# Kernel optimization log

Hardware: AMD Instinct MI355X
Metric: run time of the kernel (lower is better)

The kernel has to match this reference:

```python
import jax, jax.numpy as jnp
import numpy as np
import math

D = 256; H = 8; L = 6; DK = D // H

def _ln(x, g, b):
    m = jnp.mean(x, -1, keepdims=True)
    v = jnp.mean((x - m) ** 2, -1, keepdims=True)
    return (x - m) * jax.lax.rsqrt(v + 1e-5) * g + b

def setup_inputs() -> dict:
    key = jax.random.key(0)
    ks = jax.random.split(key, 16)
    B, N, F, E = 8, 768, 128, 4
    s = 0.02
    inp = {}
    inp['node_feats'] = jax.random.normal(ks[0], (B, N, F), jnp.float32)
    inp['adj'] = jax.random.randint(ks[1], (B, N, N), 0, 2, jnp.int32)
    inp['dist'] = jax.random.uniform(ks[2], (B, N, N), jnp.float32)
    inp['edge_type_oh'] = jax.random.uniform(ks[3], (B, N, N, E), jnp.float32)
    inp['node_proj_w'] = jax.random.normal(ks[4], (F, D), jnp.float32) * s
    inp['node_proj_b'] = jnp.zeros((D,), jnp.float32)
    inp['cls'] = jax.random.normal(ks[5], (1, 1, D), jnp.float32) * s
    inp['etw'] = jax.random.normal(ks[6], (E,), jnp.float32) * s
    inp['noedge_bias'] = jnp.float32(-2.0)
    inp['deg_scale'] = jnp.float32(0.2)
    inp['gamma'] = jnp.float32(0.8)
    inp['v2n'] = jnp.float32(0.1)
    inp['n2v'] = jnp.float32(0.1)
    inp['vself'] = jnp.float32(0.05)
    inp['ln1_g'] = jnp.ones((L, D), jnp.float32); inp['ln1_b'] = jnp.zeros((L, D), jnp.float32)
    inp['qw'] = jax.random.normal(ks[7], (L, D, D), jnp.float32) * s; inp['qb'] = jnp.zeros((L, D), jnp.float32)
    inp['kw'] = jax.random.normal(ks[8], (L, D, D), jnp.float32) * s; inp['kb'] = jnp.zeros((L, D), jnp.float32)
    inp['vw'] = jax.random.normal(ks[9], (L, D, D), jnp.float32) * s; inp['vb'] = jnp.zeros((L, D), jnp.float32)
    inp['ow'] = jax.random.normal(ks[10], (L, D, D), jnp.float32) * s; inp['ob'] = jnp.zeros((L, D), jnp.float32)
    inp['ln2_g'] = jnp.ones((L, D), jnp.float32); inp['ln2_b'] = jnp.zeros((L, D), jnp.float32)
    Dm = int(D * 1.0)  # mlp_ratio=1.0
    inp['fc1w'] = jax.random.normal(ks[11], (L, D, Dm), jnp.float32) * s; inp['fc1b'] = jnp.zeros((L, Dm), jnp.float32)
    inp['fc2w'] = jax.random.normal(ks[12], (L, Dm, D), jnp.float32) * s; inp['fc2b'] = jnp.zeros((L, D), jnp.float32)
    return inp

def _build_bias(adj_f, dist, edge_type_oh, etw, noedge_bias, deg_scale, gamma, v2n, n2v, vself):
    # DynamicAttnBiasBuilder: hard_mask=False, use_degree=True, vnode_spd_mode='replace', gamma != 0
    B, N, _ = adj_f.shape
    T = N + 1
    e = jnp.einsum('bije,e->bij', edge_type_oh, etw) - gamma * dist  # (B,N,N)
    e = jnp.where(adj_f > 0, e, e + noedge_bias)
    deg = adj_f.sum(-1)  # (B,N)
    deg_norm = (deg[:, :, None] + deg[:, None, :]) / (deg.max(axis=1, keepdims=True)[:, :, None] + 1e-6)
    e = e + deg_scale * deg_norm
    bias = jnp.zeros((B, T, T), jnp.float32)
    bias = bias.at[:, 1:, 1:].set(e)
    bias = bias.at[:, 0, 1:].set(v2n)   # vnode_spd_mode == 'replace'
    bias = bias.at[:, 1:, 0].set(n2v)
    bias = bias.at[:, 0, 0].set(vself)
    return bias  # (B,T,T), broadcast over heads

def _mhsa(x, bias, qw, qb, kw, kb, vw, vb, ow, ob):
    B, T, _ = x.shape
    q = (x @ qw + qb).reshape(B, T, H, DK).transpose(0, 2, 1, 3)
    k = (x @ kw + kb).reshape(B, T, H, DK).transpose(0, 2, 1, 3)
    v = (x @ vw + vb).reshape(B, T, H, DK).transpose(0, 2, 1, 3)
    scores = jnp.einsum('bhqd,bhkd->bhqk', q, k) / math.sqrt(DK)
    scores = scores + bias[:, None, :, :]
    attn = jax.nn.softmax(scores, axis=-1)
    out = jnp.einsum('bhqk,bhkd->bhqd', attn, v)
    out = out.transpose(0, 2, 1, 3).reshape(B, T, D)
    return out @ ow + ob

def _forward(node_feats, adj, dist, edge_type_oh, node_proj_w, node_proj_b, cls,
             etw, noedge_bias, deg_scale, gamma, v2n, n2v, vself,
             ln1_g, ln1_b, qw, qb, kw, kb, vw, vb, ow, ob,
             ln2_g, ln2_b, fc1w, fc1b, fc2w, fc2b):
    adj_f = adj.astype(jnp.float32)
    bias = _build_bias(adj_f, dist, edge_type_oh, etw, noedge_bias, deg_scale, gamma, v2n, n2v, vself)
    B = node_feats.shape[0]
    x = node_feats @ node_proj_w + node_proj_b  # (B,N,D)
    x = jnp.concatenate([jnp.broadcast_to(cls, (B, 1, D)), x], axis=1)  # prepend virtual node -> (B,T,D)
    for l in range(L):
        h = _mhsa(_ln(x, ln1_g[l], ln1_b[l]), bias, qw[l], qb[l], kw[l], kb[l], vw[l], vb[l], ow[l], ob[l])
        x = x + h
        m = _ln(x, ln2_g[l], ln2_b[l])
        m = jax.nn.gelu(m @ fc1w[l] + fc1b[l], approximate=False) @ fc2w[l] + fc2b[l]
        x = x + m
    return x

def reference(node_feats, adj, dist, edge_type_oh, node_proj_w, node_proj_b, cls,
              etw, noedge_bias, deg_scale, gamma, v2n, n2v, vself,
              ln1_g, ln1_b, qw, qb, kw, kb, vw, vb, ow, ob,
              ln2_g, ln2_b, fc1w, fc1b, fc2w, fc2b):
    return _forward(node_feats, adj, dist, edge_type_oh, node_proj_w, node_proj_b, cls,
                    etw, noedge_bias, deg_scale, gamma, v2n, n2v, vself,
                    ln1_g, ln1_b, qw, qb, kw, kb, vw, vb, ow, ob,
                    ln2_g, ln2_b, fc1w, fc1b, fc2w, fc2b)
```

## Files before the change

kernel.cpp:

```cpp
#include <hip/hip_runtime.h>
#include <math.h>

#define BB 8
#define NN 768
#define TT 769
#define DD 256
#define HH 8
#define DKK 32
#define FF 128
#define LL 6
#define MM 6152
#define SCALE 0.17677669529663687f
#define TP 832
#define KQP 784
#define KHS (KQP * DKK)
#define GBP 776
#define HP 264
#define WSZ 65536
#define NPK ((size_t)BB * 49 * 13 * 1024)

typedef __attribute__((ext_vector_type(8))) short s16x8;
typedef __attribute__((ext_vector_type(8))) unsigned short u16x8;
typedef __attribute__((ext_vector_type(4))) float f32x4;

__device__ inline short f2bf(float x) {
    unsigned u = __float_as_uint(x);
    unsigned r = (u + 0x7FFFu + ((u >> 16) & 1u)) >> 16;
    return (short)r;
}
__device__ inline float bf2f(unsigned short s) {
    return __uint_as_float(((unsigned)s) << 16);
}
__device__ inline float gelu_f(float x) {
    return 0.5f * x * (1.f + erff(x * 0.70710678118654752f));
}

__global__ __launch_bounds__(256) void deg_kernel(const int* __restrict__ adj,
                                                  float* __restrict__ deg) {
    int row  = blockIdx.x * 4 + (threadIdx.x >> 6);
    int lane = threadIdx.x & 63;
    const int* p = adj + (size_t)row * NN;
    int s = 0;
#pragma unroll
    for (int i = 0; i < NN / 64; ++i) s += p[lane + 64 * i];
#pragma unroll
    for (int off = 32; off > 0; off >>= 1) s += __shfl_xor(s, off);
    if (lane == 0) deg[row] = (float)s;
}

__global__ __launch_bounds__(256) void degmax_kernel(const float* __restrict__ deg,
                                                     float* __restrict__ dmax) {
    __shared__ float red[256];
    int b = blockIdx.x, t = threadIdx.x;
    float m = 0.f;
    for (int i = t; i < NN; i += 256) m = fmaxf(m, deg[b * NN + i]);
    red[t] = m;
    __syncthreads();
    for (int s = 128; s > 0; s >>= 1) {
        if (t < s) red[t] = fmaxf(red[t], red[t + s]);
        __syncthreads();
    }
    if (t == 0) dmax[b] = red[0];
}

__global__ __launch_bounds__(256) void bias_kernel(
    const float* __restrict__ dist, const float* __restrict__ eoh,
    const int* __restrict__ adj, const float* __restrict__ deg,
    const float* __restrict__ dmax, const float* __restrict__ etw,
    const float* __restrict__ noedge, const float* __restrict__ degsc,
    const float* __restrict__ gamma, const float* __restrict__ v2n,
    const float* __restrict__ n2v, const float* __restrict__ vself,
    unsigned short* __restrict__ bias)
{
    long long idx = (long long)blockIdx.x * 256 + threadIdx.x;
    const long long total = (long long)BB * TT * GBP;
    if (idx >= total) return;
    int b  = (int)(idx / ((long long)TT * GBP));
    int r  = (int)(idx % ((long long)TT * GBP));
    int qi = r / GBP, kj = r % GBP;
    float out;
    if (kj >= TT)                out = 0.f;
    else if (qi == 0 && kj == 0) out = vself[0];
    else if (qi == 0)            out = v2n[0];
    else if (kj == 0)            out = n2v[0];
    else {
        int i = qi - 1, j = kj - 1;
        size_t e = ((size_t)b * NN + i) * NN + j;
        float4 oh = *(const float4*)(eoh + 4 * e);
        float val = oh.x * etw[0] + oh.y * etw[1] + oh.z * etw[2] + oh.w * etw[3]
                    - gamma[0] * dist[e];
        if (adj[e] == 0) val += noedge[0];
        val += degsc[0] * (deg[b * NN + i] + deg[b * NN + j]) / (dmax[b] + 1e-6f);
        out = val;
    }
    bias[idx] = (unsigned short)f2bf(out);
}

__global__ __launch_bounds__(256) void biaspk_kernel(
    const unsigned short* __restrict__ bias, unsigned short* __restrict__ bpk)
{
    int idx = blockIdx.x * 256 + threadIdx.x;
    int jj   = idx & 7;
    int lane = (idx >> 3) & 63;
    int half = (idx >> 9) & 1;
    int c    = (idx >> 10) % 13;
    int qtb  = idx / (13 * 1024);
    int b = qtb / 49, qt = qtb - b * 49;
    int quad = lane >> 4, m16 = lane & 15;
    int j = half * 8 + jj, s = j >> 2, r = j & 3;
    int kj = c * 64 + s * 16 + m16; if (kj >= TT) kj = 0;
    int qi = qt * 16 + quad * 4 + r; if (qi >= TT) qi = TT - 1;
    bpk[idx] = bias[(size_t)(b * TT + qi) * GBP + kj];
}

__global__ __launch_bounds__(256) void nodeproj_ln_kernel(
    const float* __restrict__ nf, const float* __restrict__ w,
    const float* __restrict__ bsv, const float* __restrict__ cls,
    const float* __restrict__ g, const float* __restrict__ bvec,
    float* __restrict__ x, short* __restrict__ xn)
{
    __shared__ float sf[FF];
    __shared__ float red[256];
    int row = blockIdx.x, t = threadIdx.x;
    int b = row / TT, tr = row % TT;
    float y;
    if (tr == 0) {
        y = cls[t];
    } else {
        if (t < FF) sf[t] = nf[((size_t)b * NN + tr - 1) * FF + t];
        __syncthreads();
        y = bsv[t];
#pragma unroll 8
        for (int kk = 0; kk < FF; ++kk) y = fmaf(sf[kk], w[kk * DD + t], y);
    }
    x[(size_t)row * DD + t] = y;
    red[t] = y;
    __syncthreads();
    for (int s = 128; s > 0; s >>= 1) { if (t < s) red[t] += red[t + s]; __syncthreads(); }
    float mean = red[0] * (1.f / DD);
    __syncthreads();
    float d = y - mean;
    red[t] = d * d;
    __syncthreads();
    for (int s = 128; s > 0; s >>= 1) { if (t < s) red[t] += red[t + s]; __syncthreads(); }
    float var = red[0] * (1.f / DD);
    xn[(size_t)row * DD + t] = f2bf(d * rsqrtf(var + 1e-5f) * g[t] + bvec[t]);
}

__global__ __launch_bounds__(256) void wtrans_kernel(
    const float* __restrict__ qw, const float* __restrict__ kw,
    const float* __restrict__ vw, const float* __restrict__ ow,
    const float* __restrict__ f1w, const float* __restrict__ f2w,
    short* __restrict__ wt2)
{
    int mi = blockIdx.x >> 4, kg = blockIdx.x & 15;
    int fam = mi / 6, l = mi % 6;
    const float* W;
    if      (fam == 0) W = qw;
    else if (fam == 1) W = kw;
    else if (fam == 2) W = vw;
    else if (fam == 3) W = ow;
    else if (fam == 4) W = f1w;
    else               W = f2w;
    W += (size_t)l * DD * DD;
    int n = threadIdx.x;
    short* out = wt2 + (size_t)mi * WSZ;
#pragma unroll
    for (int kk = 0; kk < 16; ++kk) {
        int k = kg * 16 + kk;
        float val = W[(size_t)k * DD + n];
        size_t idx = (size_t)(((n >> 4) * 8 + (k >> 5)) * 512
                   + (((k >> 3) & 3) * 16 + (n & 15)) * 8 + (k & 7));
        out[idx] = f2bf(val);
    }
}

__global__ __launch_bounds__(256) void gemm_qkv_kernel(
    const short* __restrict__ A, const short* __restrict__ wtl,
    const float* __restrict__ qb, const float* __restrict__ kb,
    const float* __restrict__ vb,
    short* __restrict__ qh, short* __restrict__ kh, short* __restrict__ vtb)
{
    int t = threadIdx.x;
    int w = t >> 6, lane = t & 63, quad = lane >> 4, m16 = lane & 15;
    int bx = blockIdx.x;
    int bb = bx & 7, qt = bx >> 3;
    int fam = blockIdx.y;
    const short* Wf = wtl + (size_t)fam * 6 * WSZ;
    const float* bsv = fam == 0 ? qb : (fam == 1 ? kb : vb);
    int tpa = qt * 16 + m16; if (tpa >= TT) tpa = TT - 1;
    const short* ap = A + (size_t)(bb * TT + tpa) * DD + quad * 8;
    const short* wbase = Wf + (size_t)(w * 4) * 4096 + lane * 8;
    f32x4 acc[4] = {};
#pragma unroll
    for (int kc = 0; kc < 8; ++kc) {
        s16x8 af = *(const s16x8*)(ap + kc * 32);
#pragma unroll
        for (int nt = 0; nt < 4; ++nt) {
            s16x8 bf = *(const s16x8*)(wbase + (size_t)nt * 4096 + kc * 512);
            acc[nt] = __builtin_amdgcn_mfma_f32_16x16x32_bf16(af, bf, acc[nt], 0, 0, 0);
        }
    }
    if (fam < 2) {
        short* outp = fam == 0 ? qh : kh;
#pragma unroll
        for (int r = 0; r < 4; ++r) {
            int tpos = qt * 16 + quad * 4 + r;
            if (tpos < TT) {
                size_t rb = ((size_t)bb * HH * KQP + tpos) * DKK;
#pragma unroll
                for (int nt = 0; nt < 4; ++nt) {
                    int col = w * 64 + nt * 16 + m16;
                    float bv = bsv[col];
                    int h = col >> 5, dk = col & 31;
                    outp[rb + (size_t)h * KHS + dk] = f2bf(acc[nt][r] + bv);
                }
            }
        }
    } else {
#pragma unroll
        for (int nt = 0; nt < 4; ++nt) {
            int col = w * 64 + nt * 16 + m16;
            float bv = bsv[col];
            int h = col >> 5, dk = col & 31;
#pragma unroll
            for (int r = 0; r < 4; ++r) {
                int tpos = qt * 16 + quad * 4 + r;
                if (tpos < TT)
                    vtb[(((size_t)(bb * HH + h)) * DKK + dk) * TP + tpos] =
                        f2bf(acc[nt][r] + bv);
            }
        }
    }
}

__global__ __launch_bounds__(512) void mega_kernel(
    const short* __restrict__ q, const short* __restrict__ k,
    const short* __restrict__ vt, const unsigned short* __restrict__ bpk,
    const short* __restrict__ Wo, const short* __restrict__ W1,
    const short* __restrict__ W2,
    const float* __restrict__ ob, const float* __restrict__ g2,
    const float* __restrict__ b2, const float* __restrict__ f1b,
    const float* __restrict__ f2b, float* __restrict__ x,
    short* __restrict__ xn, const float* __restrict__ g1,
    const float* __restrict__ b1, int donext)
{
    __shared__ short Pb[8][16][72];
    __shared__ short xa[16][HP];
    __shared__ short xnl[16][HP];
    __shared__ short hb[16][HP];
    __shared__ float redS[16][8], redQ[16][8];

    int t = threadIdx.x;
    int w = t >> 6, lane = t & 63;
    int quad = lane >> 4, m16 = lane & 15;
    int bx = blockIdx.x;
    int b = bx & 7;
    int qt = bx >> 3;
    int h = w;
    int q0 = qt * 16;
    size_t qtb13 = (size_t)(b * 49 + qt) * 13;

    int qrow = q0 + m16;
    int qc = qrow < TT ? qrow : TT - 1;
    const short* qbase = q + (size_t)(b * HH + h) * KHS;
    s16x8 qa = *(const s16x8*)(qbase + (size_t)qc * DKK + quad * 8);

    const short* kbase = k + (size_t)(b * HH + h) * KHS;
    const short* vbase = vt + (((size_t)(b * HH + h)) * DKK) * TP;

    s16x8 kfA[4], kfB[4], vfA[4], vfB[4];
    u16x8 bbA0, bbA1, bbB0, bbB1;
    f32x4 sacc[4];
    f32x4 o0 = {0.f, 0.f, 0.f, 0.f};
    f32x4 o1 = {0.f, 0.f, 0.f, 0.f};
    float ls[4] = {0.f, 0.f, 0.f, 0.f};

#define LOADK_(DST, CC)                                                         \
    {                                                                           \
        _Pragma("unroll") for (int s = 0; s < 4; ++s) {                         \
            int kr = (CC) * 64 + s * 16 + m16;                                  \
            int kcl = kr < TT ? kr : TT - 1;                                    \
            DST[s] = *(const s16x8*)(kbase + (size_t)kcl * DKK + quad * 8);     \
        }                                                                       \
    }
#define LOADV_(DST, CC)                                                         \
    {                                                                           \
        int jn = (CC) * 64;                                                     \
        DST[0] = *(const s16x8*)(vbase + (size_t)m16 * TP + jn + quad * 8);     \
        DST[1] = *(const s16x8*)(vbase + (size_t)m16 * TP + jn + 32 + quad * 8);\
        DST[2] = *(const s16x8*)(vbase + (size_t)(16 + m16) * TP + jn + quad * 8);\
        DST[3] = *(const s16x8*)(vbase + (size_t)(16 + m16) * TP + jn + 32 + quad * 8);\
    }
#define LOADB_(D0, D1, CC)                                                      \
    {                                                                           \
        const unsigned short* bp_ = bpk + ((qtb13 + (CC)) << 10);               \
        D0 = *(const u16x8*)(bp_ + (lane << 3));                                \
        D1 = *(const u16x8*)(bp_ + 512 + (lane << 3));                         \
    }
#define STEP_(C, KPRE, KUSE, VUSE, VPRE, BU0, BU1, BP0, BP1, PK, PV, PBF, DOQK) \
    {                                                                           \
        if (PK)  LOADK_(KPRE, (C) + 2);                                         \
        if (PV)  LOADV_(VPRE, (C) + 1);                                         \
        if (PBF) LOADB_(BP0, BP1, (C) + 1);                                     \
        int j0 = (C) * 64;                                                      \
        _Pragma("unroll") for (int s = 0; s < 4; ++s) {                         \
            int key = j0 + s * 16 + m16;                                        \
            int kv = key < TT;                                                  \
            _Pragma("unroll") for (int r = 0; r < 4; ++r) {                     \
                int j = s * 4 + r;                                              \
                float bv = bf2f(j < 8 ? (unsigned short)BU0[j]                  \
                                      : (unsigned short)BU1[j - 8]);            \
                float sval = kv ? fmaf(sacc[s][r], SCALE, bv) : -1e30f;         \
                float p = __expf(sval - 8.0f);                                  \
                ls[r] += p;                                                     \
                Pb[w][quad * 4 + r][s * 16 + m16] = f2bf(p);                    \
            }                                                                   \
        }                                                                       \
        if (DOQK) {                                                             \
            f32x4 z = {0.f, 0.f, 0.f, 0.f};                                     \
            _Pragma("unroll") for (int s = 0; s < 4; ++s)                       \
                sacc[s] = __builtin_amdgcn_mfma_f32_16x16x32_bf16(qa, KUSE[s], z, 0, 0, 0); \
        }                                                                       \
        s16x8 pa0 = *(const s16x8*)&Pb[w][m16][quad * 8];                       \
        s16x8 pa1 = *(const s16x8*)&Pb[w][m16][32 + quad * 8];                  \
        o0 = __builtin_amdgcn_mfma_f32_16x16x32_bf16(pa0, VUSE[0], o0, 0, 0, 0);\
        o0 = __builtin_amdgcn_mfma_f32_16x16x32_bf16(pa1, VUSE[1], o0, 0, 0, 0);\
        o1 = __builtin_amdgcn_mfma_f32_16x16x32_bf16(pa0, VUSE[2], o1, 0, 0, 0);\
        o1 = __builtin_amdgcn_mfma_f32_16x16x32_bf16(pa1, VUSE[3], o1, 0, 0, 0);\
    }

    LOADK_(kfA, 0);
    LOADK_(kfB, 1);
    LOADV_(vfA, 0);
    LOADB_(bbA0, bbA1, 0);
    {
        f32x4 z = {0.f, 0.f, 0.f, 0.f};
#pragma unroll
        for (int s = 0; s < 4; ++s)
            sacc[s] = __builtin_amdgcn_mfma_f32_16x16x32_bf16(qa, kfA[s], z, 0, 0, 0);
    }

    for (int cc = 0; cc < 5; ++cc) {
        STEP_(2 * cc,     kfA, kfB, vfA, vfB, bbA0, bbA1, bbB0, bbB1, 1, 1, 1, 1)
        STEP_(2 * cc + 1, kfB, kfA, vfB, vfA, bbB0, bbB1, bbA0, bbA1, 1, 1, 1, 1)
    }
    STEP_(10, kfA, kfB, vfA, vfB, bbA0, bbA1, bbB0, bbB1, 1, 1, 1, 1)
    STEP_(11, kfB, kfA, vfB, vfA, bbB0, bbB1, bbA0, bbA1, 0, 1, 1, 1)
    STEP_(12, kfA, kfB, vfA, vfB, bbA0, bbA1, bbB0, bbB1, 0, 0, 0, 0)

#undef STEP_
#undef LOADB_
#undef LOADV_
#undef LOADK_

#pragma unroll
    for (int r = 0; r < 4; ++r) {
        float l = ls[r];
#pragma unroll
        for (int off = 1; off < 16; off <<= 1) l += __shfl_xor(l, off);
        float inv = 1.f / l;
        int rl = quad * 4 + r;
        xa[rl][h * DKK + m16]      = f2bf(o0[r] * inv);
        xa[rl][h * DKK + 16 + m16] = f2bf(o1[r] * inv);
    }
    __syncthreads();

    const short* wob = Wo + (size_t)(w * 2) * 4096 + lane * 8;
    f32x4 acco[2] = {};
#pragma unroll
    for (int kc = 0; kc < 8; ++kc) {
        s16x8 af = *(const s16x8*)&xa[m16][kc * 32 + quad * 8];
#pragma unroll
        for (int ntl = 0; ntl < 2; ++ntl) {
            s16x8 bf = *(const s16x8*)(wob + (size_t)ntl * 4096 + kc * 512);
            acco[ntl] = __builtin_amdgcn_mfma_f32_16x16x32_bf16(af, bf, acco[ntl], 0, 0, 0);
        }
    }
    float vv[2][4], sr[4], q2[4];
#pragma unroll
    for (int r = 0; r < 4; ++r) { sr[r] = 0.f; q2[r] = 0.f; }
#pragma unroll
    for (int ntl = 0; ntl < 2; ++ntl) {
        int col = w * 32 + ntl * 16 + m16;
        float bv = ob[col];
#pragma unroll
        for (int r = 0; r < 4; ++r) {
            int row = q0 + quad * 4 + r; if (row >= TT) row = TT - 1;
            float v = acco[ntl][r] + bv + x[((size_t)(b * TT + row)) * DD + col];
            vv[ntl][r] = v; sr[r] += v; q2[r] += v * v;
        }
    }
#pragma unroll
    for (int r = 0; r < 4; ++r)
#pragma unroll
        for (int off = 1; off < 16; off <<= 1) {
            sr[r] += __shfl_xor(sr[r], off);
            q2[r] += __shfl_xor(q2[r], off);
        }
    if (m16 == 0) {
#pragma unroll
        for (int r = 0; r < 4; ++r) {
            redS[quad * 4 + r][w] = sr[r];
            redQ[quad * 4 + r][w] = q2[r];
        }
    }
    __syncthreads();

#pragma unroll
    for (int r = 0; r < 4; ++r) {
        int rl = quad * 4 + r;
        float fs = 0.f, fq = 0.f;
#pragma unroll
        for (int j = 0; j < 8; ++j) { fs += redS[rl][j]; fq += redQ[rl][j]; }
        float mean = fs * (1.f / DD);
        float var = fq * (1.f / DD) - mean * mean;
        float inv = rsqrtf(var + 1e-5f);
#pragma unroll
        for (int ntl = 0; ntl < 2; ++ntl) {
            int col = w * 32 + ntl * 16 + m16;
            xnl[rl][col] = f2bf((vv[ntl][r] - mean) * inv * g2[col] + b2[col]);
        }
    }
    __syncthreads();

    const short* w1b = W1 + (size_t)(w * 2) * 4096 + lane * 8;
    f32x4 acc1[2] = {};
#pragma unroll
    for (int kc = 0; kc < 8; ++kc) {
        s16x8 af = *(const s16x8*)&xnl[m16][kc * 32 + quad * 8];
#pragma unroll
        for (int ntl = 0; ntl < 2; ++ntl) {
            s16x8 bf = *(const s16x8*)(w1b + (size_t)ntl * 4096 + kc * 512);
            acc1[ntl] = __builtin_amdgcn_mfma_f32_16x16x32_bf16(af, bf, acc1[ntl], 0, 0, 0);
        }
    }
#pragma unroll
    for (int ntl = 0; ntl < 2; ++ntl) {
        int col = w * 32 + ntl * 16 + m16;
        float fb = f1b[col];
#pragma unroll
        for (int r = 0; r < 4; ++r)
            hb[quad * 4 + r][col] = f2bf(gelu_f(acc1[ntl][r] + fb));
    }
    __syncthreads();

    const short* w2b = W2 + (size_t)(w * 2) * 4096 + lane * 8;
    f32x4 acc2[2] = {};
#pragma unroll
    for (int kc = 0; kc < 8; ++kc) {
        s16x8 af = *(const s16x8*)&hb[m16][kc * 32 + quad * 8];
#pragma unroll
        for (int ntl = 0; ntl < 2; ++ntl) {
            s16x8 bf = *(const s16x8*)(w2b + (size_t)ntl * 4096 + kc * 512);
            acc2[ntl] = __builtin_amdgcn_mfma_f32_16x16x32_bf16(af, bf, acc2[ntl], 0, 0, 0);
        }
    }
#pragma unroll
    for (int r = 0; r < 4; ++r) { sr[r] = 0.f; q2[r] = 0.f; }
#pragma unroll
    for (int ntl = 0; ntl < 2; ++ntl) {
        int col = w * 32 + ntl * 16 + m16;
        float bv = f2b[col];
#pragma unroll
        for (int r = 0; r < 4; ++r) {
            float v = acc2[ntl][r] + bv + vv[ntl][r];
            vv[ntl][r] = v; sr[r] += v; q2[r] += v * v;
        }
    }
#pragma unroll
    for (int r = 0; r < 4; ++r)
#pragma unroll
        for (int off = 1; off < 16; off <<= 1) {
            sr[r] += __shfl_xor(sr[r], off);
            q2[r] += __shfl_xor(q2[r], off);
        }
    if (m16 == 0) {
#pragma unroll
        for (int r = 0; r < 4; ++r) {
            redS[quad * 4 + r][w] = sr[r];
            redQ[quad * 4 + r][w] = q2[r];
        }
    }
    __syncthreads();

#pragma unroll
    for (int r = 0; r < 4; ++r) {
        int rl = quad * 4 + r;
        int row = q0 + rl;
        float fs = 0.f, fq = 0.f;
#pragma unroll
        for (int j = 0; j < 8; ++j) { fs += redS[rl][j]; fq += redQ[rl][j]; }
        float mean = fs * (1.f / DD);
        float var = fq * (1.f / DD) - mean * mean;
        float inv = rsqrtf(var + 1e-5f);
        if (row < TT) {
            size_t grow = (size_t)(b * TT + row) * DD;
#pragma unroll
            for (int ntl = 0; ntl < 2; ++ntl) {
                int col = w * 32 + ntl * 16 + m16;
                float v = vv[ntl][r];
                x[grow + col] = v;
                if (donext)
                    xn[grow + col] = f2bf((v - mean) * inv * g1[col] + b1[col]);
            }
        }
    }
}

extern "C" void kernel_launch(void* const* d_in, const int* in_sizes, int n_in,
                              void* d_out, int out_size, void* d_ws, size_t ws_size,
                              hipStream_t stream)
{
    const float* node_feats = (const float*)d_in[0];
    const int*   adj        = (const int*)d_in[1];
    const float* dist       = (const float*)d_in[2];
    const float* eoh        = (const float*)d_in[3];
    const float* npw        = (const float*)d_in[4];
    const float* npb        = (const float*)d_in[5];
    const float* cls        = (const float*)d_in[6];
    const float* etw        = (const float*)d_in[7];
    const float* noedge     = (const float*)d_in[8];
    const float* degsc      = (const float*)d_in[9];
    const float* gamma      = (const float*)d_in[10];
    const float* v2n        = (const float*)d_in[11];
    const float* n2v        = (const float*)d_in[12];
    const float* vself      = (const float*)d_in[13];
    const float* ln1g = (const float*)d_in[14];
    const float* ln1b = (const float*)d_in[15];
    const float* qw   = (const float*)d_in[16];
    const float* qb   = (const float*)d_in[17];
    const float* kw   = (const float*)d_in[18];
    const float* kb   = (const float*)d_in[19];
    const float* vw   = (const float*)d_in[20];
    const float* vb   = (const float*)d_in[21];
    const float* ow   = (const float*)d_in[22];
    const float* ob   = (const float*)d_in[23];
    const float* ln2g = (const float*)d_in[24];
    const float* ln2b = (const float*)d_in[25];
    const float* f1w  = (const float*)d_in[26];
    const float* f1b  = (const float*)d_in[27];
    const float* f2w  = (const float*)d_in[28];
    const float* f2b  = (const float*)d_in[29];

    float* x  = (float*)d_out;
    char* ws = (char*)d_ws;
    size_t off = 0;
    unsigned short* bias = (unsigned short*)(ws + off); off += (size_t)BB * TT * GBP * 2;
    unsigned short* bpk  = (unsigned short*)(ws + off); off += NPK * 2;
    float* deg  = (float*)(ws + off); off += (size_t)BB * NN * 4;
    float* dmax = (float*)(ws + off); off += 64;
    short* xn16 = (short*)(ws + off); off += (size_t)MM * DD * 2;
    short* qhb  = (short*)(ws + off); off += (size_t)BB * HH * KQP * DKK * 2;
    short* khb  = (short*)(ws + off); off += (size_t)BB * HH * KQP * DKK * 2;
    short* vtb  = (short*)(ws + off); off += (size_t)BB * HH * DKK * TP * 2;
    short* wt2  = (short*)(ws + off); off += (size_t)36 * WSZ * 2;

    deg_kernel<<<(BB * NN) / 4, 256, 0, stream>>>(adj, deg);
    degmax_kernel<<<BB, 256, 0, stream>>>(deg, dmax);

    long long total = (long long)BB * TT * GBP;
    bias_kernel<<<(int)((total + 255) / 256), 256, 0, stream>>>(
        dist, eoh, adj, deg, dmax, etw, noedge, degsc, gamma, v2n, n2v, vself, bias);

    biaspk_kernel<<<(int)(NPK / 256), 256, 0, stream>>>(bias, bpk);

    nodeproj_ln_kernel<<<MM, 256, 0, stream>>>(node_feats, npw, npb, cls,
                                               ln1g, ln1b, x, xn16);

    wtrans_kernel<<<576, 256, 0, stream>>>(qw, kw, vw, ow, f1w, f2w, wt2);

    dim3 gqkv(392, 3);
    gemm_qkv_kernel<<<gqkv, 256, 0, stream>>>(xn16, wt2, qb, kb, vb,
                                              qhb, khb, vtb);

    for (int l = 0; l < LL; ++l) {
        size_t bo = (size_t)l * DD;
        int donext = (l + 1 < LL) ? 1 : 0;
        size_t bn = (size_t)(l + 1 < LL ? l + 1 : 0) * DD;
        mega_kernel<<<392, 512, 0, stream>>>(
            qhb, khb, vtb, bpk,
            wt2 + (size_t)(18 + l) * WSZ,
            wt2 + (size_t)(24 + l) * WSZ,
            wt2 + (size_t)(30 + l) * WSZ,
            ob + bo, ln2g + bo, ln2b + bo, f1b + bo, f2b + bo,
            x, xn16, ln1g + bn, ln1b + bn, donext);
        if (donext)
            gemm_qkv_kernel<<<gqkv, 256, 0, stream>>>(
                xn16, wt2 + (size_t)(l + 1) * WSZ,
                qb + bn, kb + bn, vb + bn, qhb, khb, vtb);
    }
}
```

Measured before the change: 662.8 us.

## Split attention key range across two wave groups in 1024-thread mega kernel

```diff
diff --git a/kernel.cpp b/kernel.cpp
--- a/kernel.cpp
+++ b/kernel.cpp
@@ -234,7 +234,7 @@
     }
 }
 
-__global__ __launch_bounds__(512) void mega_kernel(
+__global__ __launch_bounds__(1024) void mega_kernel(
     const short* __restrict__ q, const short* __restrict__ k,
     const short* __restrict__ vt, const unsigned short* __restrict__ bpk,
     const short* __restrict__ Wo, const short* __restrict__ W1,
@@ -245,11 +245,11 @@
     short* __restrict__ xn, const float* __restrict__ g1,
     const float* __restrict__ b1, int donext)
 {
-    __shared__ short Pb[8][16][72];
+    __shared__ short Pb[16][16][72];
     __shared__ short xa[16][HP];
     __shared__ short xnl[16][HP];
     __shared__ short hb[16][HP];
-    __shared__ float redS[16][8], redQ[16][8];
+    __shared__ float redS[16][16], redQ[16][16];
 
     int t = threadIdx.x;
     int w = t >> 6, lane = t & 63;
@@ -257,9 +257,12 @@
     int bx = blockIdx.x;
     int b = bx & 7;
     int qt = bx >> 3;
-    int h = w;
+    int h = w & 7;
+    int half = w >> 3;
     int q0 = qt * 16;
     size_t qtb13 = (size_t)(b * 49 + qt) * 13;
+    int c0 = half * 7;
+    int c1 = 7 + half * 6;
 
     int qrow = q0 + m16;
     int qc = qrow < TT ? qrow : TT - 1;
@@ -330,10 +333,10 @@
         o1 = __builtin_amdgcn_mfma_f32_16x16x32_bf16(pa1, VUSE[3], o1, 0, 0, 0);\
     }
 
-    LOADK_(kfA, 0);
-    LOADK_(kfB, 1);
-    LOADV_(vfA, 0);
-    LOADB_(bbA0, bbA1, 0);
+    LOADK_(kfA, c0);
+    LOADK_(kfB, c0 + 1);
+    LOADV_(vfA, c0);
+    LOADB_(bbA0, bbA1, c0);
     {
         f32x4 z = {0.f, 0.f, 0.f, 0.f};
 #pragma unroll
@@ -341,54 +344,69 @@
             sacc[s] = __builtin_amdgcn_mfma_f32_16x16x32_bf16(qa, kfA[s], z, 0, 0, 0);
     }
 
-    for (int cc = 0; cc < 5; ++cc) {
-        STEP_(2 * cc,     kfA, kfB, vfA, vfB, bbA0, bbA1, bbB0, bbB1, 1, 1, 1, 1)
-        STEP_(2 * cc + 1, kfB, kfA, vfB, vfA, bbB0, bbB1, bbA0, bbA1, 1, 1, 1, 1)
-    }
-    STEP_(10, kfA, kfB, vfA, vfB, bbA0, bbA1, bbB0, bbB1, 1, 1, 1, 1)
-    STEP_(11, kfB, kfA, vfB, vfA, bbB0, bbB1, bbA0, bbA1, 0, 1, 1, 1)
-    STEP_(12, kfA, kfB, vfA, vfB, bbA0, bbA1, bbB0, bbB1, 0, 0, 0, 0)
+    for (int cc = 0; cc < 3; ++cc) {
+        int ca = c0 + 2 * cc;
+        STEP_(ca, kfA, kfB, vfA, vfB, bbA0, bbA1, bbB0, bbB1,
+              (ca + 2) < c1, (ca + 1) < c1, (ca + 1) < c1, (ca + 1) < c1)
+        int cb = ca + 1;
+        STEP_(cb, kfB, kfA, vfB, vfA, bbB0, bbB1, bbA0, bbA1,
+              (cb + 2) < c1, (cb + 1) < c1, (cb + 1) < c1, (cb + 1) < c1)
+    }
+    {
+        int cf = c0 + 6;
+        if (cf < c1)
+            STEP_(cf, kfA, kfB, vfA, vfB, bbA0, bbA1, bbB0, bbB1, 0, 0, 0, 0)
+    }
 
 #undef STEP_
 #undef LOADB_
 #undef LOADV_
 #undef LOADK_
 
-#pragma unroll
-    for (int r = 0; r < 4; ++r) {
-        float l = ls[r];
-#pragma unroll
-        for (int off = 1; off < 16; off <<= 1) l += __shfl_xor(l, off);
-        float inv = 1.f / l;
-        int rl = quad * 4 + r;
-        xa[rl][h * DKK + m16]      = f2bf(o0[r] * inv);
-        xa[rl][h * DKK + 16 + m16] = f2bf(o1[r] * inv);
-    }
-    __syncthreads();
-
-    const short* wob = Wo + (size_t)(w * 2) * 4096 + lane * 8;
-    f32x4 acco[2] = {};
+    __syncthreads();
+    float* pf = (float*)&Pb[0][0][0];
+    if (half == 1) {
+        float* p = pf + (size_t)(h * 64 + lane) * 13;
+        p[0] = o0[0]; p[1] = o0[1]; p[2]  = o0[2]; p[3]  = o0[3];
+        p[4] = o1[0]; p[5] = o1[1]; p[6]  = o1[2]; p[7]  = o1[3];
+        p[8] = ls[0]; p[9] = ls[1]; p[10] = ls[2]; p[11] = ls[3];
+    }
+    __syncthreads();
+    if (half == 0) {
+        const float* p = pf + (size_t)(h * 64 + lane) * 13;
+        o0[0] += p[0]; o0[1] += p[1]; o0[2] += p[2];  o0[3] += p[3];
+        o1[0] += p[4]; o1[1] += p[5]; o1[2] += p[6];  o1[3] += p[7];
+        ls[0] += p[8]; ls[1] += p[9]; ls[2] += p[10]; ls[3] += p[11];
+#pragma unroll
+        for (int r = 0; r < 4; ++r) {
+            float l = ls[r];
+#pragma unroll
+            for (int off = 1; off < 16; off <<= 1) l += __shfl_xor(l, off);
+            float inv = 1.f / l;
+            int rl = quad * 4 + r;
+            xa[rl][h * DKK + m16]      = f2bf(o0[r] * inv);
+            xa[rl][h * DKK + 16 + m16] = f2bf(o1[r] * inv);
+        }
+    }
+    __syncthreads();
+
+    const short* wob = Wo + (size_t)w * 4096 + lane * 8;
+    f32x4 acco = {};
 #pragma unroll
     for (int kc = 0; kc < 8; ++kc) {
         s16x8 af = *(const s16x8*)&xa[m16][kc * 32 + quad * 8];
-#pragma unroll
-        for (int ntl = 0; ntl < 2; ++ntl) {
-            s16x8 bf = *(const s16x8*)(wob + (size_t)ntl * 4096 + kc * 512);
-            acco[ntl] = __builtin_amdgcn_mfma_f32_16x16x32_bf16(af, bf, acco[ntl], 0, 0, 0);
-        }
-    }
-    float vv[2][4], sr[4], q2[4];
-#pragma unroll
-    for (int r = 0; r < 4; ++r) { sr[r] = 0.f; q2[r] = 0.f; }
-#pragma unroll
-    for (int ntl = 0; ntl < 2; ++ntl) {
-        int col = w * 32 + ntl * 16 + m16;
-        float bv = ob[col];
+        s16x8 bf = *(const s16x8*)(wob + kc * 512);
+        acco = __builtin_amdgcn_mfma_f32_16x16x32_bf16(af, bf, acco, 0, 0, 0);
+    }
+    int col = w * 16 + m16;
+    float vv[4], sr[4], q2[4];
+    {
+        float bvo = ob[col];
 #pragma unroll
         for (int r = 0; r < 4; ++r) {
             int row = q0 + quad * 4 + r; if (row >= TT) row = TT - 1;
-            float v = acco[ntl][r] + bv + x[((size_t)(b * TT + row)) * DD + col];
-            vv[ntl][r] = v; sr[r] += v; q2[r] += v * v;
+            float v = acco[r] + bvo + x[((size_t)(b * TT + row)) * DD + col];
+            vv[r] = v; sr[r] = v; q2[r] = v * v;
         }
     }
 #pragma unroll
@@ -412,60 +430,44 @@
         int rl = quad * 4 + r;
         float fs = 0.f, fq = 0.f;
 #pragma unroll
-        for (int j = 0; j < 8; ++j) { fs += redS[rl][j]; fq += redQ[rl][j]; }
+        for (int j = 0; j < 16; ++j) { fs += redS[rl][j]; fq += redQ[rl][j]; }
         float mean = fs * (1.f / DD);
         float var = fq * (1.f / DD) - mean * mean;
         float inv = rsqrtf(var + 1e-5f);
-#pragma unroll
-        for (int ntl = 0; ntl < 2; ++ntl) {
-            int col = w * 32 + ntl * 16 + m16;
-            xnl[rl][col] = f2bf((vv[ntl][r] - mean) * inv * g2[col] + b2[col]);
-        }
-    }
-    __syncthreads();
-
-    const short* w1b = W1 + (size_t)(w * 2) * 4096 + lane * 8;
-    f32x4 acc1[2] = {};
+        xnl[rl][col] = f2bf((vv[r] - mean) * inv * g2[col] + b2[col]);
+    }
+    __syncthreads();
+
+    const short* w1b = W1 + (size_t)w * 4096 + lane * 8;
+    f32x4 acc1 = {};
 #pragma unroll
     for (int kc = 0; kc < 8; ++kc) {
         s16x8 af = *(const s16x8*)&xnl[m16][kc * 32 + quad * 8];
-#pragma unroll
-        for (int ntl = 0; ntl < 2; ++ntl) {
-            s16x8 bf = *(const s16x8*)(w1b + (size_t)ntl * 4096 + kc * 512);
-            acc1[ntl] = __builtin_amdgcn_mfma_f32_16x16x32_bf16(af, bf, acc1[ntl], 0, 0, 0);
-        }
-    }
-#pragma unroll
-    for (int ntl = 0; ntl < 2; ++ntl) {
-        int col = w * 32 + ntl * 16 + m16;
+        s16x8 bf = *(const s16x8*)(w1b + kc * 512);
+        acc1 = __builtin_amdgcn_mfma_f32_16x16x32_bf16(af, bf, acc1, 0, 0, 0);
+    }
+    {
         float fb = f1b[col];
 #pragma unroll
         for (int r = 0; r < 4; ++r)
-            hb[quad * 4 + r][col] = f2bf(gelu_f(acc1[ntl][r] + fb));
-    }
-    __syncthreads();
-
-    const short* w2b = W2 + (size_t)(w * 2) * 4096 + lane * 8;
-    f32x4 acc2[2] = {};
+            hb[quad * 4 + r][col] = f2bf(gelu_f(acc1[r] + fb));
+    }
+    __syncthreads();
+
+    const short* w2b = W2 + (size_t)w * 4096 + lane * 8;
+    f32x4 acc2 = {};
 #pragma unroll
     for (int kc = 0; kc < 8; ++kc) {
         s16x8 af = *(const s16x8*)&hb[m16][kc * 32 + quad * 8];
-#pragma unroll
-        for (int ntl = 0; ntl < 2; ++ntl) {
-            s16x8 bf = *(const s16x8*)(w2b + (size_t)ntl * 4096 + kc * 512);
-            acc2[ntl] = __builtin_amdgcn_mfma_f32_16x16x32_bf16(af, bf, acc2[ntl], 0, 0, 0);
-        }
-    }
-#pragma unroll
-    for (int r = 0; r < 4; ++r) { sr[r] = 0.f; q2[r] = 0.f; }
-#pragma unroll
-    for (int ntl = 0; ntl < 2; ++ntl) {
-        int col = w * 32 + ntl * 16 + m16;
-        float bv = f2b[col];
+        s16x8 bf = *(const s16x8*)(w2b + kc * 512);
+        acc2 = __builtin_amdgcn_mfma_f32_16x16x32_bf16(af, bf, acc2, 0, 0, 0);
+    }
+    {
+        float bvf = f2b[col];
 #pragma unroll
         for (int r = 0; r < 4; ++r) {
-            float v = acc2[ntl][r] + bv + vv[ntl][r];
-            vv[ntl][r] = v; sr[r] += v; q2[r] += v * v;
+            float v = acc2[r] + bvf + vv[r];
+            vv[r] = v; sr[r] = v; q2[r] = v * v;
         }
     }
 #pragma unroll
@@ -490,20 +492,16 @@
         int row = q0 + rl;
         float fs = 0.f, fq = 0.f;
 #pragma unroll
-        for (int j = 0; j < 8; ++j) { fs += redS[rl][j]; fq += redQ[rl][j]; }
+        for (int j = 0; j < 16; ++j) { fs += redS[rl][j]; fq += redQ[rl][j]; }
         float mean = fs * (1.f / DD);
         float var = fq * (1.f / DD) - mean * mean;
         float inv = rsqrtf(var + 1e-5f);
         if (row < TT) {
             size_t grow = (size_t)(b * TT + row) * DD;
-#pragma unroll
-            for (int ntl = 0; ntl < 2; ++ntl) {
-                int col = w * 32 + ntl * 16 + m16;
-                float v = vv[ntl][r];
-                x[grow + col] = v;
-                if (donext)
-                    xn[grow + col] = f2bf((v - mean) * inv * g1[col] + b1[col]);
-            }
+            float v = vv[r];
+            x[grow + col] = v;
+            if (donext)
+                xn[grow + col] = f2bf((v - mean) * inv * g1[col] + b1[col]);
         }
     }
 }
@@ -578,7 +576,7 @@
         size_t bo = (size_t)l * DD;
         int donext = (l + 1 < LL) ? 1 : 0;
         size_t bn = (size_t)(l + 1 < LL ? l + 1 : 0) * DD;
-        mega_kernel<<<392, 512, 0, stream>>>(
+        mega_kernel<<<392, 1024, 0, stream>>>(
             qhb, khb, vtb, bpk,
             wt2 + (size_t)(18 + l) * WSZ,
             wt2 + (size_t)(24 + l) * WSZ,
```

New measurement: 1.274 ms. 1.92x slower.
